# Performance work log

Hardware: AMD Instinct MI355X
Metric: run time of the kernel (lower is better)

Reference implementation:

```python
import jax, jax.numpy as jnp
import numpy as np

B, S, E, H = 4, 2048, 1024, 16
DK = E // H  # 64


def setup_inputs() -> dict:
    key = jax.random.key(0)
    ks = jax.random.split(key, 11)
    s_in = 1.0 / np.sqrt(E)
    return {
        "query": jax.random.normal(ks[0], (B, S, E), jnp.float32),
        "key_": jax.random.normal(ks[1], (B, S, E), jnp.float32),
        "value": jax.random.normal(ks[2], (B, S, E), jnp.float32),
        # nn.Linear weights stored as [out, in]; applied as x @ W.T + b
        "Wq": jax.random.uniform(ks[3], (E, E), jnp.float32, -s_in, s_in),
        "bq": jax.random.uniform(ks[4], (E,), jnp.float32, -s_in, s_in),
        "Wk": jax.random.uniform(ks[5], (E, E), jnp.float32, -s_in, s_in),
        "bk": jax.random.uniform(ks[6], (E,), jnp.float32, -s_in, s_in),
        "Wv": jax.random.uniform(ks[7], (E, E), jnp.float32, -s_in, s_in),
        "bv": jax.random.uniform(ks[8], (E,), jnp.float32, -s_in, s_in),
        "Wo": jax.random.uniform(ks[9], (E, E), jnp.float32, -s_in, s_in),
        "bo": jax.random.uniform(ks[10], (E,), jnp.float32, -s_in, s_in),
    }


def reference(query, key_, value, Wq, bq, Wk, bk, Wv, bv, Wo, bo):
    scale = 1.0 / np.sqrt(DK).astype(np.float32)
    Q = query @ Wq.T + bq   # [B,S,E]
    K = key_ @ Wk.T + bk
    V = value @ Wv.T + bv
    # split heads: [B,S,H,DK] (slicing dim -1 into contiguous per-head chunks)
    Qh = Q.reshape(B, S, H, DK)
    Kh = K.reshape(B, S, H, DK)
    Vh = V.reshape(B, S, H, DK)
    scores = jnp.einsum('bqhd,bkhd->bhqk', Qh, Kh) * scale  # [B,H,S,S]
    probs = jax.nn.softmax(scores, axis=-1)
    ctx = jnp.einsum('bhqk,bkhd->bqhd', probs, Vh).reshape(B, S, E)
    out = ctx @ Wo.T + bo
    return out
```

## Files before the change

kernel.cpp:

```cpp
#include <hip/hip_runtime.h>
#include <stdint.h>
#include <stddef.h>

constexpr int BB = 4, SS = 2048, EE = 1024, HH = 16, DKH = 64;
constexpr int MM = BB * SS;
constexpr float SM_SCALE_LOG2 = 0.18033688011112042f;

typedef unsigned short u16;
typedef __attribute__((ext_vector_type(8))) short bf16x8;
typedef __attribute__((ext_vector_type(8))) unsigned short u16x8;
typedef __attribute__((ext_vector_type(4))) float f32x4;
typedef __attribute__((ext_vector_type(16))) float f32x16;
typedef __attribute__((ext_vector_type(2))) unsigned int u32x2;
typedef __attribute__((ext_vector_type(4))) unsigned int u32x4;

__device__ __forceinline__ u16 f2bf(float f) {
  unsigned u = __builtin_bit_cast(unsigned, f);
  u += 0x7FFFu + ((u >> 16) & 1u);
  return (u16)(u >> 16);
}

__device__ __forceinline__ unsigned pack2(float lo, float hi) {
  unsigned r;
  asm("v_cvt_pk_bf16_f32 %0, %1, %2" : "=v"(r) : "v"(lo), "v"(hi));
  return r;
}

__device__ __forceinline__ void gld16(const void* g, void* l) {
  __builtin_amdgcn_global_load_lds(
      (const __attribute__((address_space(1))) unsigned int*)g,
      (__attribute__((address_space(3))) unsigned int*)l, 16, 0, 0);
}

struct Cvt4 { const float* in[4]; u16* out[4]; };

__global__ void cvt_bf16_x4(Cvt4 p, int n8) {
  int i = blockIdx.x * 256 + threadIdx.x;
  if (i >= n8) return;
  const int z = blockIdx.y;
  const float4* src = (const float4*)p.in[z] + (size_t)i * 2;
  float4 a = src[0], b = src[1];
  u16x8 v;
  v[0] = f2bf(a.x); v[1] = f2bf(a.y); v[2] = f2bf(a.z); v[3] = f2bf(a.w);
  v[4] = f2bf(b.x); v[5] = f2bf(b.y); v[6] = f2bf(b.z); v[7] = f2bf(b.w);
  *((u16x8*)p.out[z] + i) = v;
}

struct GemmPtrs {
  const u16* A[3];
  const float* A32[3];
  const u16* W[3];
  const float* bias[3];
  void* C[3];
  float scale[3];
  int mode[3];
};

template <int AF32>
__global__ __launch_bounds__(256, 4) void gemm32(GemmPtrs p, int M, int N, int K) {
  __shared__ __align__(16) u16 SA[2][64 * 64];
  __shared__ __align__(16) u16 SB[2][64 * 64];
  const int t = threadIdx.x, l = t & 63, w = t >> 6;
  const int lq = l & 31, hi = l >> 5;
  const int wm = w >> 1, wn = w & 1;
  const int z = blockIdx.z;
  const u16* A = p.A[z];
  const float* Af = p.A32[z];
  const u16* W = p.W[z];
  const float* bias = p.bias[z];

  const int nwg = gridDim.x * gridDim.y;
  const int o = blockIdx.y * gridDim.x + blockIdx.x;
  const int sw = (o & 7) * (nwg >> 3) + (o >> 3);
  const int n0 = (sw % gridDim.x) * 128;
  const int m0 = (sw / gridDim.x) * 128;

  f32x16 acc[2][2];
#pragma unroll
  for (int i = 0; i < 2; ++i)
#pragma unroll
    for (int j = 0; j < 2; ++j)
#pragma unroll
      for (int r = 0; r < 16; ++r) acc[i][j][r] = 0.f;

  auto stageB = [&](int buf, int kt) {
#pragma unroll
    for (int i = 0; i < 2; ++i) {
      const int ci = i * 256 + t;
      const int r = ci >> 3, P = ci & 7;
      const int L = P ^ (r & 7);
      const int mr = r + ((L & 4) << 4);
      const int kc = L & 3;
      gld16(W + (size_t)(n0 + mr) * K + kt * 32 + kc * 8,
            (char*)&SB[buf][0] + (i * 256 + (t & ~63)) * 16);
    }
  };
  auto stageAb = [&](int buf, int kt) {
#pragma unroll
    for (int i = 0; i < 2; ++i) {
      const int ci = i * 256 + t;
      const int r = ci >> 3, P = ci & 7;
      const int L = P ^ (r & 7);
      const int mr = r + ((L & 4) << 4);
      const int kc = L & 3;
      gld16(A + (size_t)(m0 + mr) * K + kt * 32 + kc * 8,
            (char*)&SA[buf][0] + (i * 256 + (t & ~63)) * 16);
    }
  };
  float4 av[2][2];
  auto loadAf = [&](int kt) {
#pragma unroll
    for (int i = 0; i < 2; ++i) {
      const int u = i * 256 + t;
      const int mr = u >> 2, kc = u & 3;
      const float4* src = (const float4*)(Af + (size_t)(m0 + mr) * K + kt * 32 + kc * 8);
      av[i][0] = src[0];
      av[i][1] = src[1];
    }
  };
  auto writeAf = [&](int buf) {
#pragma unroll
    for (int i = 0; i < 2; ++i) {
      const int u = i * 256 + t;
      const int mr = u >> 2, kc = u & 3;
      const int r = mr & 63;
      const int P = (((mr >> 6) << 2) + kc) ^ (r & 7);
      u32x4 pk;
      pk[0] = pack2(av[i][0].x, av[i][0].y);
      pk[1] = pack2(av[i][0].z, av[i][0].w);
      pk[2] = pack2(av[i][1].x, av[i][1].y);
      pk[3] = pack2(av[i][1].z, av[i][1].w);
      *(u32x4*)((char*)&SA[buf][0] + r * 128 + P * 16) = pk;
    }
  };

  if (AF32) {
    loadAf(0);
    writeAf(0);
  } else {
    stageAb(0, 0);
  }
  stageB(0, 0);
  __syncthreads();

  int cur = 0;
  const int NT = K >> 5;
  const int lsw = lq & 7;
  for (int kt = 0; kt < NT; ++kt) {
    const bool nx = (kt + 1 < NT);
    if (nx) {
      if (AF32) loadAf(kt + 1);
      else stageAb(cur ^ 1, kt + 1);
      stageB(cur ^ 1, kt + 1);
    }
    const u16* Ac = &SA[cur][0];
    const u16* Bc = &SB[cur][0];
    __builtin_amdgcn_s_setprio(1);
#pragma unroll
    for (int ks = 0; ks < 2; ++ks) {
      const int ca = ((wm << 2) + (ks << 1) + hi) ^ lsw;
      const int cb = ((wn << 2) + (ks << 1) + hi) ^ lsw;
      bf16x8 a0 = *(const bf16x8*)(Ac + lq * 64 + ca * 8);
      bf16x8 a1 = *(const bf16x8*)(Ac + (32 + lq) * 64 + ca * 8);
      bf16x8 b0 = *(const bf16x8*)(Bc + lq * 64 + cb * 8);
      bf16x8 b1 = *(const bf16x8*)(Bc + (32 + lq) * 64 + cb * 8);
      acc[0][0] = __builtin_amdgcn_mfma_f32_32x32x16_bf16(a0, b0, acc[0][0], 0, 0, 0);
      acc[0][1] = __builtin_amdgcn_mfma_f32_32x32x16_bf16(a0, b1, acc[0][1], 0, 0, 0);
      acc[1][0] = __builtin_amdgcn_mfma_f32_32x32x16_bf16(a1, b0, acc[1][0], 0, 0, 0);
      acc[1][1] = __builtin_amdgcn_mfma_f32_32x32x16_bf16(a1, b1, acc[1][1], 0, 0, 0);
    }
    __builtin_amdgcn_s_setprio(0);
    if (AF32 && nx) {
      __builtin_amdgcn_sched_barrier(0);
      writeAf(cur ^ 1);
    }
    __syncthreads();
    cur ^= 1;
  }

  const float sc = p.scale[z];
  const int mode = p.mode[z];
#pragma unroll
  for (int fr = 0; fr < 2; ++fr) {
#pragma unroll
    for (int fc = 0; fc < 2; ++fc) {
      const int col = n0 + wn * 64 + fc * 32 + lq;
      const float bv = bias[col];
#pragma unroll
      for (int g = 0; g < 4; ++g) {
        const int mb = m0 + wm * 64 + fr * 32 + 8 * g + 4 * hi;
        float v[4];
#pragma unroll
        for (int j = 0; j < 4; ++j) v[j] = (acc[fr][fc][4 * g + j] + bv) * sc;
        if (mode == 1) {
#pragma unroll
          for (int j = 0; j < 4; ++j)
            ((float*)p.C[z])[(size_t)(mb + j) * N + col] = v[j];
        } else if (mode == 0) {
#pragma unroll
          for (int j = 0; j < 4; ++j)
            ((u16*)p.C[z])[(size_t)(mb + j) * N + col] = f2bf(v[j]);
        } else {
          const int b = mb >> 11, s = mb & 2047;
          u16* dst = (u16*)p.C[z] +
                     ((size_t)((b * 16 + (col >> 6)) * 64 + (col & 63))) * SS + s;
          uint2 pk;
          pk.x = pack2(v[0], v[1]);
          pk.y = pack2(v[2], v[3]);
          *(uint2*)dst = pk;
        }
      }
    }
  }
}

__global__ __launch_bounds__(256, 4) void attn_fwd3(const u16* __restrict__ Q,
                                                    const u16* __restrict__ K,
                                                    const u16* __restrict__ Vt,
                                                    u16* __restrict__ C) {
  __shared__ __align__(16) u16 Ks[2][64 * 64];
  __shared__ __align__(16) u16 Vs[2][64 * 64];

  const int t = threadIdx.x, l = t & 63, w = t >> 6;
  const int lq = l & 31, hi = l >> 5;
  const int q0 = blockIdx.x * 128;
  const int bh = blockIdx.y, bb = bh >> 4, hh = bh & 15;

  const u16* qp = Q + ((size_t)(bb * SS + q0 + w * 32 + lq)) * EE + hh * 64 + hi * 8;
  bf16x8 qf[4];
  qf[0] = *(const bf16x8*)(qp);
  qf[1] = *(const bf16x8*)(qp + 16);
  qf[2] = *(const bf16x8*)(qp + 32);
  qf[3] = *(const bf16x8*)(qp + 48);

  const u16* Kbase = K + (size_t)bb * SS * EE + hh * 64;
  const u16* Vbase = Vt + (size_t)bh * DKH * SS;

  f32x16 accA, accB;
  f32x16 z16;
#pragma unroll
  for (int i = 0; i < 16; ++i) { accA[i] = 0.f; accB[i] = 0.f; z16[i] = 0.f; }
  float lsum = 0.0f;

  auto stage = [&](int buf, int kt) {
#pragma unroll
    for (int i = 0; i < 2; ++i) {
      const int slot = i * 256 + t;
      const int row = slot >> 3, pc = slot & 7;
      const int lc = pc ^ (row & 7);
      const int lbyte = (i * 256 + (t & ~63)) * 16;
      gld16(Kbase + (size_t)(kt * 64 + row) * EE + lc * 8, (char*)&Ks[buf][0] + lbyte);
      gld16(Vbase + (size_t)row * SS + kt * 64 + lc * 8, (char*)&Vs[buf][0] + lbyte);
    }
  };

  auto mkfrag = [&](const f32x16& p, int base) -> bf16x8 {
    unsigned A0 = pack2(p[base + 0], p[base + 1]);
    unsigned A1 = pack2(p[base + 2], p[base + 3]);
    unsigned B0 = pack2(p[base + 4], p[base + 5]);
    unsigned B1 = pack2(p[base + 6], p[base + 7]);
    u32x2 r0 = __builtin_amdgcn_permlane32_swap(A0, B0, false, false);
    u32x2 r1 = __builtin_amdgcn_permlane32_swap(A1, B1, false, false);
    u32x4 fr;
    fr[0] = r0[0]; fr[1] = r1[0]; fr[2] = r0[1]; fr[3] = r1[1];
    return __builtin_bit_cast(bf16x8, fr);
  };

  stage(0, 0);
  __syncthreads();
  int cur = 0;
  for (int kt = 0; kt < SS / 64; ++kt) {
    if (kt + 1 < SS / 64) stage(cur ^ 1, kt + 1);
    const u16* Kc = &Ks[cur][0];
    const u16* Vc = &Vs[cur][0];

    f32x16 s0, s1;
    __builtin_amdgcn_s_setprio(1);
    {
      const int c = hi ^ (lq & 7);
      bf16x8 kf0 = *(const bf16x8*)(Kc + lq * 64 + c * 8);
      bf16x8 kf1 = *(const bf16x8*)(Kc + (32 + lq) * 64 + c * 8);
      s0 = __builtin_amdgcn_mfma_f32_32x32x16_bf16(kf0, qf[0], z16, 0, 0, 0);
      s1 = __builtin_amdgcn_mfma_f32_32x32x16_bf16(kf1, qf[0], z16, 0, 0, 0);
    }
#pragma unroll
    for (int m = 1; m < 4; ++m) {
      const int c = (2 * m + hi) ^ (lq & 7);
      bf16x8 kf0 = *(const bf16x8*)(Kc + lq * 64 + c * 8);
      bf16x8 kf1 = *(const bf16x8*)(Kc + (32 + lq) * 64 + c * 8);
      s0 = __builtin_amdgcn_mfma_f32_32x32x16_bf16(kf0, qf[m], s0, 0, 0, 0);
      s1 = __builtin_amdgcn_mfma_f32_32x32x16_bf16(kf1, qf[m], s1, 0, 0, 0);
    }
    __builtin_amdgcn_s_setprio(0);

#pragma unroll
    for (int i = 0; i < 16; ++i) {
      s0[i] = __builtin_amdgcn_exp2f(s0[i]);
      s1[i] = __builtin_amdgcn_exp2f(s1[i]);
    }
    float sa = 0.f, sb = 0.f, sc2 = 0.f, sd = 0.f;
#pragma unroll
    for (int i = 0; i < 8; ++i) {
      sa += s0[i]; sb += s0[i + 8];
      sc2 += s1[i]; sd += s1[i + 8];
    }
    lsum += (sa + sb) + (sc2 + sd);

    bf16x8 pf[4];
    pf[0] = mkfrag(s0, 0);
    pf[1] = mkfrag(s0, 8);
    pf[2] = mkfrag(s1, 0);
    pf[3] = mkfrag(s1, 8);

    __builtin_amdgcn_s_setprio(1);
#pragma unroll
    for (int s = 0; s < 4; ++s) {
      const int c = (2 * s + hi) ^ (lq & 7);
      bf16x8 vf0 = *(const bf16x8*)(Vc + lq * 64 + c * 8);
      bf16x8 vf1 = *(const bf16x8*)(Vc + (32 + lq) * 64 + c * 8);
      accA = __builtin_amdgcn_mfma_f32_32x32x16_bf16(vf0, pf[s], accA, 0, 0, 0);
      accB = __builtin_amdgcn_mfma_f32_32x32x16_bf16(vf1, pf[s], accB, 0, 0, 0);
    }
    __builtin_amdgcn_s_setprio(0);
    __syncthreads();
    cur ^= 1;
  }

  const float inv = 1.0f / (lsum + __shfl_xor(lsum, 32));
  char* Tw = (char*)&Ks[0][0] + w * 4096;
#pragma unroll
  for (int g = 0; g < 4; ++g) {
    uint2 pa, pb;
    pa.x = pack2(accA[4 * g + 0] * inv, accA[4 * g + 1] * inv);
    pa.y = pack2(accA[4 * g + 2] * inv, accA[4 * g + 3] * inv);
    pb.x = pack2(accB[4 * g + 0] * inv, accB[4 * g + 1] * inv);
    pb.y = pack2(accB[4 * g + 2] * inv, accB[4 * g + 3] * inv);
    const int sub = 8 * hi, sw = (lq & 7) << 4;
    *(uint2*)(Tw + lq * 128 + (((g) << 4) ^ sw) + sub) = pa;
    *(uint2*)(Tw + lq * 128 + (((4 + g) << 4) ^ sw) + sub) = pb;
  }
  const int qr0 = l >> 3, ch = l & 7;
#pragma unroll
  for (int ps = 0; ps < 4; ++ps) {
    const int qr = ps * 8 + qr0;
    u32x4 vv = *(const u32x4*)(Tw + qr * 128 + ((ch ^ (qr & 7)) << 4));
    u16* dst = C + ((size_t)(bb * SS + q0 + w * 32 + qr)) * EE + hh * 64 + ch * 8;
    *(u32x4*)dst = vv;
  }
}

extern "C" void kernel_launch(void* const* d_in, const int* in_sizes, int n_in,
                              void* d_out, int out_size, void* d_ws, size_t ws_size,
                              hipStream_t stream) {
  (void)in_sizes; (void)n_in; (void)out_size; (void)ws_size;
  const float* query = (const float*)d_in[0];
  const float* key_  = (const float*)d_in[1];
  const float* value = (const float*)d_in[2];
  const float* Wq = (const float*)d_in[3];
  const float* bq = (const float*)d_in[4];
  const float* Wk = (const float*)d_in[5];
  const float* bk = (const float*)d_in[6];
  const float* Wv = (const float*)d_in[7];
  const float* bv = (const float*)d_in[8];
  const float* Wo = (const float*)d_in[9];
  const float* bo = (const float*)d_in[10];

  char* ws = (char*)d_ws;
  const size_t SZX = (size_t)MM * EE * 2;
  const size_t SZW = (size_t)EE * EE * 2;
  u16* Qb  = (u16*)(ws + 0 * SZX);
  u16* Kb  = (u16*)(ws + 1 * SZX);
  u16* Vtb = (u16*)(ws + 2 * SZX);
  u16* Cb  = (u16*)(ws + 3 * SZX);
  u16* Wqb = (u16*)(ws + 4 * SZX + 0 * SZW);
  u16* Wkb = (u16*)(ws + 4 * SZX + 1 * SZW);
  u16* Wvb = (u16*)(ws + 4 * SZX + 2 * SZW);
  u16* Wob = (u16*)(ws + 4 * SZX + 3 * SZW);

  const int n8w = EE * EE / 8;

  Cvt4 cw{};
  cw.in[0] = Wq; cw.in[1] = Wk; cw.in[2] = Wv; cw.in[3] = Wo;
  cw.out[0] = Wqb; cw.out[1] = Wkb; cw.out[2] = Wvb; cw.out[3] = Wob;
  cvt_bf16_x4<<<dim3(n8w / 256, 4), 256, 0, stream>>>(cw, n8w);

  GemmPtrs g{};
  g.A32[0] = query; g.A32[1] = key_; g.A32[2] = value;
  g.W[0] = Wqb; g.W[1] = Wkb; g.W[2] = Wvb;
  g.bias[0] = bq; g.bias[1] = bk; g.bias[2] = bv;
  g.C[0] = Qb; g.C[1] = Kb; g.C[2] = Vtb;
  g.scale[0] = SM_SCALE_LOG2; g.scale[1] = 1.0f; g.scale[2] = 1.0f;
  g.mode[0] = 0; g.mode[1] = 0; g.mode[2] = 2;
  gemm32<1><<<dim3(EE / 128, MM / 128, 3), 256, 0, stream>>>(g, MM, EE, EE);

  attn_fwd3<<<dim3(SS / 128, BB * HH), 256, 0, stream>>>(Qb, Kb, Vtb, Cb);

  GemmPtrs g2{};
  g2.A[0] = Cb; g2.W[0] = Wob; g2.bias[0] = bo; g2.C[0] = d_out;
  g2.scale[0] = 1.0f; g2.mode[0] = 1;
  gemm32<0><<<dim3(EE / 128, MM / 128, 1), 256, 0, stream>>>(g2, MM, EE, EE);
}
```

Before: 217.4 us.

## Stage fp32 activations directly into LDS and convert to bf16 at fragment load

The QKV projection GEMM used to load fp32 activations into registers, pack them to bf16 and write them to LDS after the MFMAs. It now copies the fp32 tiles asynchronously with direct global-to-LDS loads into a swizzled fp32 buffer and converts to bf16 when reading fragments. This removes the register round trip and its serialization after compute, so A loads overlap fully with the MFMAs. In exchange LDS use grows to 48KB dynamic for that kernel, launch bounds drop to 3 waves per SIMD, and each k-step does more LDS traffic plus repeated conversion work.

```diff
diff --git a/kernel.cpp b/kernel.cpp
--- a/kernel.cpp
+++ b/kernel.cpp
@@ -57,14 +57,16 @@
 };
 
 template <int AF32>
-__global__ __launch_bounds__(256, 4) void gemm32(GemmPtrs p, int M, int N, int K) {
-  __shared__ __align__(16) u16 SA[2][64 * 64];
-  __shared__ __align__(16) u16 SB[2][64 * 64];
+__global__ __launch_bounds__(256, 3) void gemm32(GemmPtrs p, int M, int N, int K) {
+  extern __shared__ __align__(16) char smem[];
+  float* SAf = (float*)smem;
+  u16* SAb = (u16*)smem;
+  u16* SB = (u16*)(smem + (AF32 ? 32768 : 16384));
   const int t = threadIdx.x, l = t & 63, w = t >> 6;
   const int lq = l & 31, hi = l >> 5;
   const int wm = w >> 1, wn = w & 1;
   const int z = blockIdx.z;
-  const u16* A = p.A[z];
+  const u16* Ab = p.A[z];
   const float* Af = p.A32[z];
   const u16* W = p.W[z];
   const float* bias = p.bias[z];
@@ -83,97 +85,98 @@
 #pragma unroll
       for (int r = 0; r < 16; ++r) acc[i][j][r] = 0.f;
 
-  auto stageB = [&](int buf, int kt) {
+  auto stage = [&](int buf, int kt) {
+    if (AF32) {
+#pragma unroll
+      for (int i = 0; i < 4; ++i) {
+        const int ci = i * 256 + t;
+        const int r = ci >> 3, P = ci & 7;
+        const int L = P ^ (r & 7);
+        gld16(Af + (size_t)(m0 + r) * K + kt * 32 + L * 4,
+              (char*)(SAf + buf * 128 * 32) + (i * 256 + (t & ~63)) * 16);
+      }
+    } else {
+#pragma unroll
+      for (int i = 0; i < 2; ++i) {
+        const int ci = i * 256 + t;
+        const int r = ci >> 3, P = ci & 7;
+        const int L = P ^ (r & 7);
+        const int m = r + ((L & 4) << 4);
+        const int kc = L & 3;
+        gld16(Ab + (size_t)(m0 + m) * K + kt * 32 + kc * 8,
+              (char*)(SAb + buf * 64 * 64) + (i * 256 + (t & ~63)) * 16);
+      }
+    }
 #pragma unroll
     for (int i = 0; i < 2; ++i) {
       const int ci = i * 256 + t;
       const int r = ci >> 3, P = ci & 7;
       const int L = P ^ (r & 7);
-      const int mr = r + ((L & 4) << 4);
+      const int m = r + ((L & 4) << 4);
       const int kc = L & 3;
-      gld16(W + (size_t)(n0 + mr) * K + kt * 32 + kc * 8,
-            (char*)&SB[buf][0] + (i * 256 + (t & ~63)) * 16);
+      gld16(W + (size_t)(n0 + m) * K + kt * 32 + kc * 8,
+            (char*)(SB + buf * 64 * 64) + (i * 256 + (t & ~63)) * 16);
     }
   };
-  auto stageAb = [&](int buf, int kt) {
-#pragma unroll
-    for (int i = 0; i < 2; ++i) {
-      const int ci = i * 256 + t;
-      const int r = ci >> 3, P = ci & 7;
-      const int L = P ^ (r & 7);
-      const int mr = r + ((L & 4) << 4);
-      const int kc = L & 3;
-      gld16(A + (size_t)(m0 + mr) * K + kt * 32 + kc * 8,
-            (char*)&SA[buf][0] + (i * 256 + (t & ~63)) * 16);
-    }
-  };
-  float4 av[2][2];
-  auto loadAf = [&](int kt) {
-#pragma unroll
-    for (int i = 0; i < 2; ++i) {
-      const int u = i * 256 + t;
-      const int mr = u >> 2, kc = u & 3;
-      const float4* src = (const float4*)(Af + (size_t)(m0 + mr) * K + kt * 32 + kc * 8);
-      av[i][0] = src[0];
-      av[i][1] = src[1];
-    }
-  };
-  auto writeAf = [&](int buf) {
-#pragma unroll
-    for (int i = 0; i < 2; ++i) {
-      const int u = i * 256 + t;
-      const int mr = u >> 2, kc = u & 3;
-      const int r = mr & 63;
-      const int P = (((mr >> 6) << 2) + kc) ^ (r & 7);
-      u32x4 pk;
-      pk[0] = pack2(av[i][0].x, av[i][0].y);
-      pk[1] = pack2(av[i][0].z, av[i][0].w);
-      pk[2] = pack2(av[i][1].x, av[i][1].y);
-      pk[3] = pack2(av[i][1].z, av[i][1].w);
-      *(u32x4*)((char*)&SA[buf][0] + r * 128 + P * 16) = pk;
-    }
-  };
-
-  if (AF32) {
-    loadAf(0);
-    writeAf(0);
-  } else {
-    stageAb(0, 0);
-  }
-  stageB(0, 0);
+
+  stage(0, 0);
   __syncthreads();
-
   int cur = 0;
   const int NT = K >> 5;
   const int lsw = lq & 7;
   for (int kt = 0; kt < NT; ++kt) {
-    const bool nx = (kt + 1 < NT);
-    if (nx) {
-      if (AF32) loadAf(kt + 1);
-      else stageAb(cur ^ 1, kt + 1);
-      stageB(cur ^ 1, kt + 1);
-    }
-    const u16* Ac = &SA[cur][0];
-    const u16* Bc = &SB[cur][0];
+    if (kt + 1 < NT) stage(cur ^ 1, kt + 1);
+
+    bf16x8 a0[2], a1[2], b0[2], b1[2];
+    if (AF32) {
+      const float* Ac = SAf + cur * 128 * 32;
+#pragma unroll
+      for (int ks = 0; ks < 2; ++ks) {
+#pragma unroll
+        for (int fi = 0; fi < 2; ++fi) {
+          const int R = wm * 64 + fi * 32 + lq;
+          const char* rowp = (const char*)(Ac + (size_t)R * 32);
+          const int L0 = 4 * ks + 2 * hi;
+          const f32x4 v0 = *(const f32x4*)(rowp + ((L0 ^ (R & 7)) * 16));
+          const f32x4 v1 = *(const f32x4*)(rowp + (((L0 + 1) ^ (R & 7)) * 16));
+          u32x4 pk;
+          pk[0] = pack2(v0[0], v0[1]);
+          pk[1] = pack2(v0[2], v0[3]);
+          pk[2] = pack2(v1[0], v1[1]);
+          pk[3] = pack2(v1[2], v1[3]);
+          const bf16x8 af = __builtin_bit_cast(bf16x8, pk);
+          if (fi == 0) a0[ks] = af;
+          else a1[ks] = af;
+        }
+      }
+    } else {
+      const u16* Ac = SAb + cur * 64 * 64;
+#pragma unroll
+      for (int ks = 0; ks < 2; ++ks) {
+        const int ca = ((wm << 2) + (ks << 1) + hi) ^ lsw;
+        a0[ks] = *(const bf16x8*)(Ac + lq * 64 + ca * 8);
+        a1[ks] = *(const bf16x8*)(Ac + (32 + lq) * 64 + ca * 8);
+      }
+    }
+    {
+      const u16* Bc = SB + cur * 64 * 64;
+#pragma unroll
+      for (int ks = 0; ks < 2; ++ks) {
+        const int cb = ((wn << 2) + (ks << 1) + hi) ^ lsw;
+        b0[ks] = *(const bf16x8*)(Bc + lq * 64 + cb * 8);
+        b1[ks] = *(const bf16x8*)(Bc + (32 + lq) * 64 + cb * 8);
+      }
+    }
+
     __builtin_amdgcn_s_setprio(1);
 #pragma unroll
     for (int ks = 0; ks < 2; ++ks) {
-      const int ca = ((wm << 2) + (ks << 1) + hi) ^ lsw;
-      const int cb = ((wn << 2) + (ks << 1) + hi) ^ lsw;
-      bf16x8 a0 = *(const bf16x8*)(Ac + lq * 64 + ca * 8);
-      bf16x8 a1 = *(const bf16x8*)(Ac + (32 + lq) * 64 + ca * 8);
-      bf16x8 b0 = *(const bf16x8*)(Bc + lq * 64 + cb * 8);
-      bf16x8 b1 = *(const bf16x8*)(Bc + (32 + lq) * 64 + cb * 8);
-      acc[0][0] = __builtin_amdgcn_mfma_f32_32x32x16_bf16(a0, b0, acc[0][0], 0, 0, 0);
-      acc[0][1] = __builtin_amdgcn_mfma_f32_32x32x16_bf16(a0, b1, acc[0][1], 0, 0, 0);
-      acc[1][0] = __builtin_amdgcn_mfma_f32_32x32x16_bf16(a1, b0, acc[1][0], 0, 0, 0);
-      acc[1][1] = __builtin_amdgcn_mfma_f32_32x32x16_bf16(a1, b1, acc[1][1], 0, 0, 0);
+      acc[0][0] = __builtin_amdgcn_mfma_f32_32x32x16_bf16(a0[ks], b0[ks], acc[0][0], 0, 0, 0);
+      acc[0][1] = __builtin_amdgcn_mfma_f32_32x32x16_bf16(a0[ks], b1[ks], acc[0][1], 0, 0, 0);
+      acc[1][0] = __builtin_amdgcn_mfma_f32_32x32x16_bf16(a1[ks], b0[ks], acc[1][0], 0, 0, 0);
+      acc[1][1] = __builtin_amdgcn_mfma_f32_32x32x16_bf16(a1[ks], b1[ks], acc[1][1], 0, 0, 0);
     }
     __builtin_amdgcn_s_setprio(0);
-    if (AF32 && nx) {
-      __builtin_amdgcn_sched_barrier(0);
-      writeAf(cur ^ 1);
-    }
     __syncthreads();
     cur ^= 1;
   }
@@ -391,12 +394,12 @@
   g.C[0] = Qb; g.C[1] = Kb; g.C[2] = Vtb;
   g.scale[0] = SM_SCALE_LOG2; g.scale[1] = 1.0f; g.scale[2] = 1.0f;
   g.mode[0] = 0; g.mode[1] = 0; g.mode[2] = 2;
-  gemm32<1><<<dim3(EE / 128, MM / 128, 3), 256, 0, stream>>>(g, MM, EE, EE);
+  gemm32<1><<<dim3(EE / 128, MM / 128, 3), 256, 49152, stream>>>(g, MM, EE, EE);
 
   attn_fwd3<<<dim3(SS / 128, BB * HH), 256, 0, stream>>>(Qb, Kb, Vtb, Cb);
 
   GemmPtrs g2{};
   g2.A[0] = Cb; g2.W[0] = Wob; g2.bias[0] = bo; g2.C[0] = d_out;
   g2.scale[0] = 1.0f; g2.mode[0] = 1;
-  gemm32<0><<<dim3(EE / 128, MM / 128, 1), 256, 0, stream>>>(g2, MM, EE, EE);
-}
+  gemm32<0><<<dim3(EE / 128, MM / 128, 1), 256, 32768, stream>>>(g2, MM, EE, EE);
+}
```

After: 197.7 us (median of 4 runs). 9.1% less time.
